# Kernel optimization log

Measured on AMD Instinct MI355X. Metric: run time of the kernel, lower is better.

## Reference

```python
import jax, jax.numpy as jnp
import numpy as np

IN_FEATURES = 4096
OUT_FEATURES = 14336
TILE = 16
BITS = 3
HAD = 128  # Hadamard block size used by EXL3 rotations


def _hadamard_matrix(n):
    H = np.array([[1.0]], dtype=np.float64)
    while H.shape[0] < n:
        H = np.block([[H, H], [H, -H]])
    return H

H128 = jnp.asarray(_hadamard_matrix(HAD) / np.sqrt(HAD), dtype=jnp.float32)


def had128(v):
    # blockwise normalized Hadamard transform over the last axis
    s = v.shape
    return (v.reshape(s[:-1] + (s[-1] // HAD, HAD)) @ H128).reshape(s)


def dequant_trellis(trellis):
    # trellis: [Tk, Tn, 48] uint16. Each 16x16 tile holds 256 weights coded as a
    # tail-biting trellis bitstream of 256*3 = 768 bits (48 uint16 words).
    # Weight i's 16-bit state is the circular bit window [3i, 3i+16).
    u = trellis.astype(jnp.uint32)  # [Tk, Tn, 48]
    i = jnp.arange(TILE * TILE)  # 256 weights per tile
    b = i * BITS                 # bit offset of each state
    w = b // 16                  # word index
    r = (b % 16).astype(jnp.uint32)
    hi = u[..., w]               # [Tk, Tn, 256]
    lo = u[..., (w + 1) % 48]
    comb = (hi << 16) | lo       # 32-bit window starting at word w
    states = (comb >> (jnp.uint32(16) - r)) & jnp.uint32(0xFFFF)
    # QTIP-style 3INST decode: LCG, exponent mask, sum of two fp16 bitcasts
    z = states * jnp.uint32(89226354) + jnp.uint32(64248484)
    z = z & jnp.uint32(0x8FFF8FFF)
    lo16 = jax.lax.bitcast_convert_type((z & jnp.uint32(0xFFFF)).astype(jnp.uint16), jnp.float16)
    hi16 = jax.lax.bitcast_convert_type((z >> 16).astype(jnp.uint16), jnp.float16)
    vals = lo16.astype(jnp.float32) + hi16.astype(jnp.float32)  # [Tk, Tn, 256]
    Tk, Tn = trellis.shape[0], trellis.shape[1]
    W = vals.reshape(Tk, Tn, TILE, TILE).transpose(0, 2, 1, 3).reshape(Tk * TILE, Tn * TILE)
    return W  # [K, N] float32


def setup_inputs() -> dict:
    key = jax.random.key(0)
    k1, k2, k3, k4, k5 = jax.random.split(key, 5)
    x = jax.random.normal(k1, (8, IN_FEATURES), dtype=jnp.float16)
    trellis = jax.random.randint(
        k2, (IN_FEATURES // TILE, OUT_FEATURES // TILE, 48), 0, 65536, dtype=jnp.int32
    ).astype(jnp.uint16)
    suh = jax.random.normal(k3, (IN_FEATURES,), dtype=jnp.float16)
    svh = jax.random.normal(k4, (OUT_FEATURES,), dtype=jnp.float16)
    bias = (jax.random.normal(k5, (OUT_FEATURES,), dtype=jnp.float16) * jnp.float16(0.01))
    return {"x": x, "trellis": trellis, "suh": suh, "svh": svh, "bias": bias}


def reference(x, trellis, suh, svh, bias):
    # EXL3 linear: y = Had( Had(x * suh) @ Wq ) * svh + bias
    W = dequant_trellis(trellis)                       # [K, N]
    xs = x.astype(jnp.float32) * suh.astype(jnp.float32)
    xh = had128(xs)                                    # input rotation
    y = xh @ W                                         # [B, N]
    yh = had128(y)                                     # output rotation
    out = yh * svh.astype(jnp.float32) + bias.astype(jnp.float32)
    return out.astype(jnp.float16)
```

## Files before the change

### kernel.cpp

```cpp
#include <hip/hip_runtime.h>
#include <hip/hip_fp16.h>
#include <hip/hip_bf16.h>
#include <stdint.h>


#define IN_F 4096
#define OUT_F 14336
#define BATCH 8
#define TN_TILES 896
#define NW 48
#define KSLICES 8
#define ITERS 16
#define RS128 0.08838834764831845f

typedef __attribute__((ext_vector_type(4))) float f32x4;
typedef __attribute__((ext_vector_type(8))) short s16x8;

__device__ __hip_bfloat16 g_xh[BATCH * IN_F];
__device__ float g_y[BATCH * OUT_F];
__device__ uint32_t g_flags[2];

__global__ void k_detect(const uint32_t* __restrict__ tr,
                         const uint32_t* __restrict__ xw) {
  int lane = threadIdx.x;
  uint32_t hi = 0;
  for (int i = lane; i < 4096; i += 64) hi |= (tr[i] >> 16);
  uint32_t low13 = 0;
  for (int i = lane; i < 256; i += 64) low13 |= (xw[i] & 0x1FFFu);
  int anyhi = __any(hi != 0);
  int anylow = __any(low13 != 0);
  if (lane == 0) {
    g_flags[0] = anyhi ? 1u : 0u;
    g_flags[1] = anylow ? 0u : 1u;
  }
}

__global__ void k_rot_in(const void* __restrict__ xp,
                         const void* __restrict__ suhp) {
  const int b = blockIdx.x;
  const int row = b >> 5, blk = b & 31;
  const int lane = threadIdx.x;
  {
    int base = b * 448;
    #pragma unroll
    for (int k = 0; k < 7; ++k) g_y[base + k * 64 + lane] = 0.f;
  }
  const uint32_t ffmt = g_flags[1];
  const int i0 = blk * 128 + lane;
  float x0, x1, s0, s1;
  if (ffmt) {
    const float* x = (const float*)xp;
    const float* sh = (const float*)suhp;
    x0 = x[row * IN_F + i0];      x1 = x[row * IN_F + i0 + 64];
    s0 = sh[i0];                  s1 = sh[i0 + 64];
  } else {
    const __hip_bfloat16* x = (const __hip_bfloat16*)xp;
    const __hip_bfloat16* sh = (const __hip_bfloat16*)suhp;
    x0 = __bfloat162float(x[row * IN_F + i0]);
    x1 = __bfloat162float(x[row * IN_F + i0 + 64]);
    s0 = __bfloat162float(sh[i0]);
    s1 = __bfloat162float(sh[i0 + 64]);
  }
  float v0 = x0 * s0 * RS128;
  float v1 = x1 * s1 * RS128;
  { float a = v0 + v1, s = v0 - v1; v0 = a; v1 = s; }
  #pragma unroll
  for (int d = 32; d >= 1; d >>= 1) {
    float w0 = __shfl_xor(v0, d);
    float w1 = __shfl_xor(v1, d);
    if (lane & d) { v0 = w0 - v0; v1 = w1 - v1; }
    else          { v0 = v0 + w0; v1 = v1 + w1; }
  }
  g_xh[row * IN_F + i0]      = __float2bfloat16(v0);
  g_xh[row * IN_F + i0 + 64] = __float2bfloat16(v1);
}

__global__ __launch_bounds__(256) void k_main(const uint32_t* __restrict__ tr) {
  __shared__ uint32_t comb[2][8][NW];
  const int t = threadIdx.x;
  const int lane = t & 63;
  const int wv = t >> 6;
  const int bx = blockIdx.x;
  const int ks = blockIdx.y;
  const uint32_t fmt = g_flags[0];
  const uint16_t* __restrict__ tr16 = (const uint16_t*)tr;

  const int q   = lane >> 4;
  const int cc  = lane & 15;
  const int r0  = (q & 1) << 3;
  const int par = q >> 1;
  const int w0  = 3 * r0 + ((3 * cc) >> 4);
  const uint32_t sh = 16u - (uint32_t)((3 * cc) & 15);

  f32x4 acc = {0.f, 0.f, 0.f, 0.f};

  auto stage = [&](int it, int buf) {
    const int tk0 = ks * 32 + it * 2;
    #pragma unroll
    for (int rep = 0; rep < 2; ++rep) {
      int idx = t + rep * 256;
      if (idx < 8 * NW) {
        int tile = idx / NW;
        int w = idx - tile * NW;
        int wvs = tile >> 1;
        int p2 = tile & 1;
        long gb = ((long)(tk0 + p2) * TN_TILES + (bx * 4 + wvs)) * NW;
        int w1 = (w + 1 == NW) ? 0 : (w + 1);
        uint32_t hiw, low;
        if (fmt) { hiw = tr16[gb + w]; low = tr16[gb + w1]; }
        else     { hiw = tr[gb + w];   low = tr[gb + w1]; }
        comb[buf][tile][w] = (hiw << 16) | low;
      }
    }
  };

  stage(0, 0);
  __syncthreads();

  for (int it = 0; it < ITERS; ++it) {
    const int cur = it & 1;
    if (it + 1 < ITERS) stage(it + 1, cur ^ 1);

    const uint32_t* cb = &comb[cur][wv * 2 + par][0];
    float val[8];
    #pragma unroll
    for (int j = 0; j < 8; ++j) {
      uint32_t cw = cb[w0 + 3 * j];
      uint32_t st = (cw >> sh) & 0xFFFFu;
      uint32_t zz = __umul24(st, 31858u) + 64248484u +
                    (__umul24(st, 1361u) << 16);
      zz &= 0x8FFF8FFFu;
      float flo = __half2float(__ushort_as_half((unsigned short)(zz & 0xFFFFu)));
      float fhi = __half2float(__ushort_as_half((unsigned short)(zz >> 16)));
      val[j] = flo + fhi;
    }
    uint32_t pk[4];
    #pragma unroll
    for (int j2 = 0; j2 < 4; ++j2) {
      uint32_t u0 = __float_as_uint(val[2 * j2]);
      uint32_t u1 = __float_as_uint(val[2 * j2 + 1]);
      u0 += 0x7FFFu + ((u0 >> 16) & 1u);
      u1 += 0x7FFFu + ((u1 >> 16) & 1u);
      pk[j2] = (u0 >> 16) | (u1 & 0xFFFF0000u);
    }
    union { uint32_t u[4]; s16x8 v; } bu;
    bu.u[0] = pk[0]; bu.u[1] = pk[1]; bu.u[2] = pk[2]; bu.u[3] = pk[3];

    const int tk0 = ks * 32 + it * 2;
    s16x8 afrag = {0, 0, 0, 0, 0, 0, 0, 0};
    if (cc < 8)
      afrag = *(const s16x8*)(g_xh + cc * IN_F + tk0 * 16 + q * 8);

    acc = __builtin_amdgcn_mfma_f32_16x16x32_bf16(afrag, bu.v, acc, 0, 0, 0);
    __syncthreads();
  }

  if (q < 2) {
    const int n = (bx * 4 + wv) * 16 + cc;
    #pragma unroll
    for (int rg = 0; rg < 4; ++rg) {
      int row = q * 4 + rg;
      atomicAdd(&g_y[row * OUT_F + n], acc[rg]);
    }
  }
}

__global__ void k_rot_out(const void* __restrict__ svhp,
                          const void* __restrict__ biasp,
                          void* __restrict__ outp) {
  const int nblk = blockIdx.x;
  const int row = blockIdx.y;
  const int lane = threadIdx.x;
  const uint32_t ffmt = g_flags[1];
  const int n0 = nblk * 128 + lane;
  float v0 = g_y[row * OUT_F + n0] * RS128;
  float v1 = g_y[row * OUT_F + n0 + 64] * RS128;
  { float a = v0 + v1, s = v0 - v1; v0 = a; v1 = s; }
  #pragma unroll
  for (int d = 32; d >= 1; d >>= 1) {
    float w0 = __shfl_xor(v0, d);
    float w1 = __shfl_xor(v1, d);
    if (lane & d) { v0 = w0 - v0; v1 = w1 - v1; }
    else          { v0 = v0 + w0; v1 = v1 + w1; }
  }
  if (ffmt) {
    const float* svh = (const float*)svhp;
    const float* bias = (const float*)biasp;
    float* out = (float*)outp;
    out[(long)row * OUT_F + n0]      = v0 * svh[n0] + bias[n0];
    out[(long)row * OUT_F + n0 + 64] = v1 * svh[n0 + 64] + bias[n0 + 64];
  } else {
    const __hip_bfloat16* svh = (const __hip_bfloat16*)svhp;
    const __hip_bfloat16* bias = (const __hip_bfloat16*)biasp;
    __hip_bfloat16* out = (__hip_bfloat16*)outp;
    out[(long)row * OUT_F + n0] = __float2bfloat16(
        v0 * __bfloat162float(svh[n0]) + __bfloat162float(bias[n0]));
    out[(long)row * OUT_F + n0 + 64] = __float2bfloat16(
        v1 * __bfloat162float(svh[n0 + 64]) + __bfloat162float(bias[n0 + 64]));
  }
}

extern "C" void kernel_launch(void* const* d_in, const int* in_sizes, int n_in,
                              void* d_out, int out_size, void* d_ws,
                              size_t ws_size, hipStream_t stream) {
  const void*     x    = d_in[0];
  const uint32_t* tr   = (const uint32_t*)d_in[1];
  const void*     suh  = d_in[2];
  const void*     svh  = d_in[3];
  const void*     bias = d_in[4];

  k_detect<<<1, 64, 0, stream>>>(tr, (const uint32_t*)x);
  k_rot_in<<<256, 64, 0, stream>>>(x, suh);
  k_main<<<dim3(TN_TILES / 4, KSLICES), 256, 0, stream>>>(tr);
  k_rot_out<<<dim3(OUT_F / 128, BATCH), 64, 0, stream>>>(svh, bias, d_out);
}
```

Measured before the change: 127.5 us.

## Per-wave trellis loading with shuffles, fp16 decode and MFMA, drop block barriers

The main kernel now has each wave load its own two trellis tiles as packed 32-bit words straight into registers. It builds the overlapping 32-bit windows with a lane shuffle and byte permute, writes them to a per-wave shared buffer, and drops the block-wide __syncthreads. Decoding adds the two halves as packed half2 and feeds an fp16 MFMA, which removes the float-to-bf16 rounding, and the input rotation is now stored as fp16. This cuts global load count, barrier stalls and ALU work per tile. It relies on wave-synchronous shared memory access without a barrier, and fp16 addition changes rounding compared with fp32 addition.

```diff
diff --git a/kernel.cpp b/kernel.cpp
--- a/kernel.cpp
+++ b/kernel.cpp
@@ -8,15 +8,14 @@
 #define OUT_F 14336
 #define BATCH 8
 #define TN_TILES 896
-#define NW 48
 #define KSLICES 8
 #define ITERS 16
 #define RS128 0.08838834764831845f
 
 typedef __attribute__((ext_vector_type(4))) float f32x4;
-typedef __attribute__((ext_vector_type(8))) short s16x8;
-
-__device__ __hip_bfloat16 g_xh[BATCH * IN_F];
+typedef __attribute__((ext_vector_type(8))) _Float16 f16x8;
+
+__device__ _Float16 g_xh[BATCH * IN_F];
 __device__ float g_y[BATCH * OUT_F];
 __device__ uint32_t g_flags[2];
 
@@ -24,9 +23,11 @@
                          const uint32_t* __restrict__ xw) {
   int lane = threadIdx.x;
   uint32_t hi = 0;
-  for (int i = lane; i < 4096; i += 64) hi |= (tr[i] >> 16);
+  #pragma unroll
+  for (int k = 0; k < 8; ++k) hi |= (tr[k * 64 + lane] >> 16);
   uint32_t low13 = 0;
-  for (int i = lane; i < 256; i += 64) low13 |= (xw[i] & 0x1FFFu);
+  #pragma unroll
+  for (int k = 0; k < 4; ++k) low13 |= (xw[k * 64 + lane] & 0x1FFFu);
   int anyhi = __any(hi != 0);
   int anylow = __any(low13 != 0);
   if (lane == 0) {
@@ -71,97 +72,88 @@
     if (lane & d) { v0 = w0 - v0; v1 = w1 - v1; }
     else          { v0 = v0 + w0; v1 = v1 + w1; }
   }
-  g_xh[row * IN_F + i0]      = __float2bfloat16(v0);
-  g_xh[row * IN_F + i0 + 64] = __float2bfloat16(v1);
+  g_xh[row * IN_F + i0]      = (_Float16)v0;
+  g_xh[row * IN_F + i0 + 64] = (_Float16)v1;
 }
 
 __global__ __launch_bounds__(256) void k_main(const uint32_t* __restrict__ tr) {
-  __shared__ uint32_t comb[2][8][NW];
+  __shared__ uint32_t comb[4][2][96];
   const int t = threadIdx.x;
   const int lane = t & 63;
   const int wv = t >> 6;
-  const int bx = blockIdx.x;
+  const int tn = blockIdx.x * 4 + wv;
   const int ks = blockIdx.y;
   const uint32_t fmt = g_flags[0];
-  const uint16_t* __restrict__ tr16 = (const uint16_t*)tr;
-
-  const int q   = lane >> 4;
-  const int cc  = lane & 15;
-  const int r0  = (q & 1) << 3;
+
+  const int m = lane & 31;
+  const int mm = (m < 24) ? m : 0;
+  const int tsel = lane >> 5;
+  const int src = (m == 23) ? (lane - 23) : (lane + 1);
+
+  const int q = lane >> 4;
+  const int cc = lane & 15;
   const int par = q >> 1;
-  const int w0  = 3 * r0 + ((3 * cc) >> 4);
-  const uint32_t sh = 16u - (uint32_t)((3 * cc) & 15);
-
-  f32x4 acc = {0.f, 0.f, 0.f, 0.f};
-
-  auto stage = [&](int it, int buf) {
-    const int tk0 = ks * 32 + it * 2;
-    #pragma unroll
-    for (int rep = 0; rep < 2; ++rep) {
-      int idx = t + rep * 256;
-      if (idx < 8 * NW) {
-        int tile = idx / NW;
-        int w = idx - tile * NW;
-        int wvs = tile >> 1;
-        int p2 = tile & 1;
-        long gb = ((long)(tk0 + p2) * TN_TILES + (bx * 4 + wvs)) * NW;
-        int w1 = (w + 1 == NW) ? 0 : (w + 1);
-        uint32_t hiw, low;
-        if (fmt) { hiw = tr16[gb + w]; low = tr16[gb + w1]; }
-        else     { hiw = tr[gb + w];   low = tr[gb + w1]; }
-        comb[buf][tile][w] = (hiw << 16) | low;
-      }
+  const int w0 = 3 * ((q & 1) << 3) + ((3 * cc) >> 4);
+  const uint32_t shr = 16u - (uint32_t)((3 * cc) & 15);
+
+  auto gload = [&](int it) -> uint32_t {
+    const int tk = ks * 32 + it * 2 + tsel;
+    const long tb = (long)tk * TN_TILES + tn;
+    if (fmt) {
+      return tr[tb * 24 + mm];
+    } else {
+      uint32_t u0 = tr[tb * 48 + 2 * mm];
+      uint32_t u1 = tr[tb * 48 + 2 * mm + 1];
+      return u0 | (u1 << 16);
     }
   };
 
-  stage(0, 0);
-  __syncthreads();
-
+  f32x4 acc = {0.f, 0.f, 0.f, 0.f};
+  uint32_t X = gload(0);
+
+  #pragma unroll 4
   for (int it = 0; it < ITERS; ++it) {
-    const int cur = it & 1;
-    if (it + 1 < ITERS) stage(it + 1, cur ^ 1);
-
-    const uint32_t* cb = &comb[cur][wv * 2 + par][0];
-    float val[8];
+    const int buf = it & 1;
+    uint32_t Y = __shfl(X, src);
+    uint32_t c0 = (X >> 16) | (X << 16);
+    uint32_t c1 = __builtin_amdgcn_perm(X, Y, 0x07060100u);
+    if (m < 24) {
+      uint32_t* cw = &comb[wv][buf][tsel * 48 + 2 * m];
+      cw[0] = c0; cw[1] = c1;
+    }
+    uint32_t Xn = (it + 1 < ITERS) ? gload(it + 1) : 0u;
+
+    const uint32_t* cb = &comb[wv][buf][par * 48 + w0];
+    union { __half2 h[4]; f16x8 v; } bfrag;
     #pragma unroll
-    for (int j = 0; j < 8; ++j) {
-      uint32_t cw = cb[w0 + 3 * j];
-      uint32_t st = (cw >> sh) & 0xFFFFu;
-      uint32_t zz = __umul24(st, 31858u) + 64248484u +
-                    (__umul24(st, 1361u) << 16);
-      zz &= 0x8FFF8FFFu;
-      float flo = __half2float(__ushort_as_half((unsigned short)(zz & 0xFFFFu)));
-      float fhi = __half2float(__ushort_as_half((unsigned short)(zz >> 16)));
-      val[j] = flo + fhi;
+    for (int g = 0; g < 4; ++g) {
+      uint32_t cw0 = cb[6 * g];
+      uint32_t cw1 = cb[6 * g + 3];
+      uint32_t st0 = (cw0 >> shr) & 0xFFFFu;
+      uint32_t st1 = (cw1 >> shr) & 0xFFFFu;
+      uint32_t z0 = __umul24(st0, 31858u) + 64248484u + (__umul24(st0, 1361u) << 16);
+      uint32_t z1 = __umul24(st1, 31858u) + 64248484u + (__umul24(st1, 1361u) << 16);
+      z0 &= 0x8FFF8FFFu; z1 &= 0x8FFF8FFFu;
+      uint32_t lo = __builtin_amdgcn_perm(z1, z0, 0x05040100u);
+      uint32_t hi = __builtin_amdgcn_perm(z1, z0, 0x07060302u);
+      __half2 ha = *(__half2*)&lo;
+      __half2 hb = *(__half2*)&hi;
+      bfrag.h[g] = __hadd2(ha, hb);
     }
-    uint32_t pk[4];
+
+    f16x8 afrag = {0, 0, 0, 0, 0, 0, 0, 0};
+    if (cc < 8)
+      afrag = *(const f16x8*)(g_xh + cc * IN_F + ks * 512 + it * 32 + q * 8);
+
+    acc = __builtin_amdgcn_mfma_f32_16x16x32_f16(afrag, bfrag.v, acc, 0, 0, 0);
+    X = Xn;
+  }
+
+  if (q < 2) {
+    const int n = tn * 16 + cc;
     #pragma unroll
-    for (int j2 = 0; j2 < 4; ++j2) {
-      uint32_t u0 = __float_as_uint(val[2 * j2]);
-      uint32_t u1 = __float_as_uint(val[2 * j2 + 1]);
-      u0 += 0x7FFFu + ((u0 >> 16) & 1u);
-      u1 += 0x7FFFu + ((u1 >> 16) & 1u);
-      pk[j2] = (u0 >> 16) | (u1 & 0xFFFF0000u);
-    }
-    union { uint32_t u[4]; s16x8 v; } bu;
-    bu.u[0] = pk[0]; bu.u[1] = pk[1]; bu.u[2] = pk[2]; bu.u[3] = pk[3];
-
-    const int tk0 = ks * 32 + it * 2;
-    s16x8 afrag = {0, 0, 0, 0, 0, 0, 0, 0};
-    if (cc < 8)
-      afrag = *(const s16x8*)(g_xh + cc * IN_F + tk0 * 16 + q * 8);
-
-    acc = __builtin_amdgcn_mfma_f32_16x16x32_bf16(afrag, bu.v, acc, 0, 0, 0);
-    __syncthreads();
-  }
-
-  if (q < 2) {
-    const int n = (bx * 4 + wv) * 16 + cc;
-    #pragma unroll
-    for (int rg = 0; rg < 4; ++rg) {
-      int row = q * 4 + rg;
-      atomicAdd(&g_y[row * OUT_F + n], acc[rg]);
-    }
+    for (int rg = 0; rg < 4; ++rg)
+      atomicAdd(&g_y[(q * 4 + rg) * OUT_F + n], acc[rg]);
   }
 }
 
```

New measurement: 108.0 us. -15.3%, faster.
